# Optimization experiments

Measured on AMD Instinct MI355X. Metric: run time of the kernel, lower is better.

The kernel has to match this reference:

```python
import jax, jax.numpy as jnp
import numpy as np

H, E, NI = 100000, 200000, 1000000
D_H, D_E, D_OUT = 128, 64, 128
LN_EPS = 1e-5


def _linear(x, W, b):
    # torch nn.Linear convention: W is [out, in]
    return x @ W.T + b


def _scatter_mean(vals, idx, num_segments):
    # scatter_mean with empty segments producing 0 (sum=0 / max(count,1))
    s = jax.ops.segment_sum(vals, idx, num_segments=num_segments)
    c = jax.ops.segment_sum(jnp.ones((vals.shape[0], 1), vals.dtype), idx,
                            num_segments=num_segments)
    return s / jnp.maximum(c, 1.0)


def setup_inputs() -> dict:
    key = jax.random.key(0)
    ks = jax.random.split(key, 16)
    inv = lambda n: 1.0 / np.sqrt(n)
    return {
        "x_h": jax.random.normal(ks[0], (H, D_H), jnp.float32),
        "h2_edge_attr": jax.random.normal(ks[1], (E, D_E), jnp.float32),
        "Wp": jax.random.uniform(ks[2], (D_OUT, D_H), jnp.float32, -inv(D_H), inv(D_H)),
        "bp": jnp.zeros((D_OUT,), jnp.float32),
        "We1": jax.random.uniform(ks[3], (D_OUT, D_H + D_E), jnp.float32, -inv(D_H + D_E), inv(D_H + D_E)),
        "be1": jnp.zeros((D_OUT,), jnp.float32),
        "We2": jax.random.uniform(ks[4], (D_OUT, D_OUT), jnp.float32, -inv(D_OUT), inv(D_OUT)),
        "be2": jnp.zeros((D_OUT,), jnp.float32),
        "Wn1": jax.random.uniform(ks[5], (D_OUT, D_OUT), jnp.float32, -inv(D_OUT), inv(D_OUT)),
        "bn1": jnp.zeros((D_OUT,), jnp.float32),
        "Wn2": jax.random.uniform(ks[6], (D_OUT, D_OUT), jnp.float32, -inv(D_OUT), inv(D_OUT)),
        "bn2": jnp.zeros((D_OUT,), jnp.float32),
        "gamma": jnp.ones((D_OUT,), jnp.float32),
        "beta": jnp.zeros((D_OUT,), jnp.float32),
        "fg_id": jax.random.randint(ks[7], (NI,), 0, H, jnp.int32),
        "res_id": jax.random.randint(ks[8], (NI,), 0, E, jnp.int32),
    }


def reference(x_h, h2_edge_attr, Wp, bp, We1, be1, We2, be2,
              Wn1, bn1, Wn2, bn2, gamma, beta, fg_id, res_id):
    # node -> edge: mean of member node features per hyperedge
    edge_node_mean = _scatter_mean(x_h[fg_id], res_id, E)            # [E, d_h]
    e_in = jnp.concatenate([edge_node_mean, h2_edge_attr], axis=-1)  # [E, d_h+d_e]
    edge_msg = _linear(jax.nn.relu(_linear(e_in, We1, be1)), We2, be2)  # [E, d_out]
    # edge -> node: mean of incident edge messages per hypernode
    node_msg = _scatter_mean(edge_msg[res_id], fg_id, H)             # [H, d_out]
    z = _linear(x_h, Wp, bp) + _linear(jax.nn.relu(_linear(node_msg, Wn1, bn1)), Wn2, bn2)
    z = jax.nn.relu(z)
    mu = jnp.mean(z, axis=-1, keepdims=True)
    var = jnp.var(z, axis=-1, keepdims=True)
    return (z - mu) * jax.lax.rsqrt(var + LN_EPS) * gamma + beta
```

## Files before the change

kernel.cpp:

```cpp
#include <hip/hip_runtime.h>

#define H_N   100000
#define E_N   200000
#define NI_N  1000000
#define LN_EPS 1e-5f

#define NBUCK_E 3125
#define NBUCK_H 1563
#define SUBCAP_E 128
#define SUBCAP_H 192
#define CAP_E 512
#define CAP_H 1024
#define BCNT_PAD 16

typedef __attribute__((ext_vector_type(8))) short bf16x8;
typedef __attribute__((ext_vector_type(4))) float floatx4;
typedef __attribute__((ext_vector_type(4))) int intx4;

__device__ inline unsigned short f2bf(float f) {
  unsigned u = __builtin_bit_cast(unsigned, f);
  u += 0x7fffu + ((u >> 16) & 1u);
  return (unsigned short)(u >> 16);
}
__device__ inline float bf2f(unsigned short s) {
  unsigned u = ((unsigned)s) << 16;
  return __builtin_bit_cast(float, u);
}
__device__ inline unsigned get_xcc() {
  unsigned x;
  asm volatile("s_getreg_b32 %0, hwreg(HW_REG_XCC_ID)" : "=s"(x));
  return x & 7;
}

__global__ __launch_bounds__(256) void k_cvt_bf16(const float4* __restrict__ src,
                                                  unsigned short* __restrict__ dst,
                                                  int n4) {
  int i = blockIdx.x * 256 + threadIdx.x;
  if (i >= n4) return;
  float4 v = src[i];
  union { unsigned short us[4]; unsigned long long u64; } p;
  p.us[0] = f2bf(v.x); p.us[1] = f2bf(v.y);
  p.us[2] = f2bf(v.z); p.us[3] = f2bf(v.w);
  *(unsigned long long*)(dst + (size_t)i * 4) = p.u64;
}

__global__ __launch_bounds__(256) void k_bucket(
    const int* __restrict__ fg, const int* __restrict__ res,
    int* __restrict__ bcnt_e, int* __restrict__ bcnt_h,
    unsigned* __restrict__ pairs_e, unsigned* __restrict__ pairs_h) {
  int i0 = (blockIdx.x * 256 + threadIdx.x) * 4;
  if (i0 >= NI_N) return;
  unsigned xcc = get_xcc();
  intx4 f4 = __builtin_nontemporal_load((const intx4*)(fg + i0));
  intx4 r4 = __builtin_nontemporal_load((const intx4*)(res + i0));
#pragma unroll
  for (int j = 0; j < 4; ++j) {
    int f = f4[j], r = r4[j];
    int be = r >> 6, se = r & 63;
    int pe = atomicAdd(bcnt_e + ((size_t)xcc * NBUCK_E + be) * BCNT_PAD, 1);
    if (pe < SUBCAP_E)
      pairs_e[((size_t)xcc * NBUCK_E + be) * SUBCAP_E + pe] =
          ((unsigned)se << 24) | (unsigned)f;
    int bh = f >> 6, sh = f & 63;
    int ph = atomicAdd(bcnt_h + ((size_t)xcc * NBUCK_H + bh) * BCNT_PAD, 1);
    if (ph < SUBCAP_H)
      pairs_h[((size_t)xcc * NBUCK_H + bh) * SUBCAP_H + ph] =
          ((unsigned)sh << 24) | (unsigned)r;
  }
}

__global__ __launch_bounds__(256, 4) void k_edge_fused(
    const unsigned short* __restrict__ xh, const short* __restrict__ attr_bf,
    const unsigned* __restrict__ pairs, const int* __restrict__ bcnt,
    const short* __restrict__ w1, const float* __restrict__ b1,
    const short* __restrict__ w2, const float* __restrict__ b2,
    unsigned short* __restrict__ edge_msg) {
  __shared__ short meanS[64][136];
  __shared__ int ubuf[4352];
  short (*h1s)[136] = (short(*)[136])ubuf;
  unsigned* raw = (unsigned*)ubuf;
  unsigned* sortedp = raw + CAP_E;
  int* cnts = (int*)(sortedp + CAP_E);
  int* curs = cnts + 65;

  const int b = blockIdx.x;
  const int t = threadIdx.x;

  int total = 0;
#pragma unroll
  for (int x = 0; x < 8; ++x) {
    int c = min(bcnt[((size_t)x * NBUCK_E + b) * BCNT_PAD], SUBCAP_E);
    const unsigned* src = pairs + ((size_t)x * NBUCK_E + b) * SUBCAP_E;
    for (int j = t; j < c; j += 256) {
      int d = total + j;
      if (d < CAP_E) raw[d] = src[j];
    }
    total += c;
  }
  const int cnt = min(total, CAP_E);
  if (t <= 64) cnts[t] = 0;
  __syncthreads();
  for (int j = t; j < cnt; j += 256)
    atomicAdd(&cnts[(raw[j] >> 24) + 1], 1);
  __syncthreads();
  for (int d = 1; d <= 64; d <<= 1) {
    int v = 0;
    if (t <= 64 && t >= d) v = cnts[t - d];
    __syncthreads();
    if (t <= 64) cnts[t] += v;
    __syncthreads();
  }
  if (t < 64) curs[t] = cnts[t];
  __syncthreads();
  for (int j = t; j < cnt; j += 256) {
    unsigned p = raw[j];
    int d = atomicAdd(&curs[p >> 24], 1);
    sortedp[d] = p & 0xFFFFFFu;
  }
  __syncthreads();

  const int wave = t >> 6, lane = t & 63;
  for (int s = wave; s < 64; s += 4) {
    int o = cnts[s], e = cnts[s + 1];
    float a0 = 0.f, a1 = 0.f;
    int j = o;
    for (; j + 1 < e; j += 2) {
      int i0 = sortedp[j], i1 = sortedp[j + 1];
      unsigned v0 = *(const unsigned*)(xh + (size_t)i0 * 128 + lane * 2);
      unsigned v1 = *(const unsigned*)(xh + (size_t)i1 * 128 + lane * 2);
      a0 += bf2f((unsigned short)(v0 & 0xffffu)) + bf2f((unsigned short)(v1 & 0xffffu));
      a1 += bf2f((unsigned short)(v0 >> 16)) + bf2f((unsigned short)(v1 >> 16));
    }
    if (j < e) {
      int i0 = sortedp[j];
      unsigned v0 = *(const unsigned*)(xh + (size_t)i0 * 128 + lane * 2);
      a0 += bf2f((unsigned short)(v0 & 0xffffu));
      a1 += bf2f((unsigned short)(v0 >> 16));
    }
    float inv = (e > o) ? 1.0f / (float)(e - o) : 0.0f;
    *(unsigned*)&meanS[s][lane * 2] =
        (unsigned)f2bf(a0 * inv) | ((unsigned)f2bf(a1 * inv) << 16);
  }
  __syncthreads();

  const int row  = lane & 15;
  const int quad = lane >> 4;
  const int e0   = b * 64;
  const int cb   = wave * 32;

  bf16x8 B1[2][6];
#pragma unroll
  for (int nl = 0; nl < 2; ++nl)
#pragma unroll
    for (int ks = 0; ks < 6; ++ks)
      B1[nl][ks] = *(const bf16x8*)(w1 + (size_t)(cb + nl * 16 + row) * 192 +
                                    ks * 32 + quad * 8);

  floatx4 acc[4][2];
#pragma unroll
  for (int m = 0; m < 4; ++m)
#pragma unroll
    for (int nl = 0; nl < 2; ++nl) acc[m][nl] = (floatx4){0.f, 0.f, 0.f, 0.f};

#pragma unroll
  for (int ks = 0; ks < 6; ++ks) {
    bf16x8 a[4];
#pragma unroll
    for (int m = 0; m < 4; ++m) {
      if (ks < 4) {
        a[m] = *(const bf16x8*)&meanS[m * 16 + row][ks * 32 + quad * 8];
      } else {
        int e = e0 + m * 16 + row;
        a[m] = *(const bf16x8*)(attr_bf + (size_t)e * 64 + (ks - 4) * 32 + quad * 8);
      }
    }
#pragma unroll
    for (int m = 0; m < 4; ++m)
#pragma unroll
      for (int nl = 0; nl < 2; ++nl)
        acc[m][nl] = __builtin_amdgcn_mfma_f32_16x16x32_bf16(a[m], B1[nl][ks],
                                                             acc[m][nl], 0, 0, 0);
  }

#pragma unroll
  for (int nl = 0; nl < 2; ++nl) {
    float bias = b1[cb + nl * 16 + row];
#pragma unroll
    for (int m = 0; m < 4; ++m)
#pragma unroll
      for (int r = 0; r < 4; ++r)
        h1s[m * 16 + quad * 4 + r][cb + nl * 16 + row] =
            (short)f2bf(fmaxf(acc[m][nl][r] + bias, 0.0f));
  }

  bf16x8 B2[2][4];
#pragma unroll
  for (int nl = 0; nl < 2; ++nl)
#pragma unroll
    for (int ks = 0; ks < 4; ++ks)
      B2[nl][ks] = *(const bf16x8*)(w2 + (size_t)(cb + nl * 16 + row) * 128 +
                                    ks * 32 + quad * 8);
  __syncthreads();

  floatx4 acc2[4][2];
#pragma unroll
  for (int m = 0; m < 4; ++m)
#pragma unroll
    for (int nl = 0; nl < 2; ++nl) acc2[m][nl] = (floatx4){0.f, 0.f, 0.f, 0.f};

#pragma unroll
  for (int ks = 0; ks < 4; ++ks) {
    bf16x8 a[4];
#pragma unroll
    for (int m = 0; m < 4; ++m)
      a[m] = *(const bf16x8*)&h1s[m * 16 + row][ks * 32 + quad * 8];
#pragma unroll
    for (int m = 0; m < 4; ++m)
#pragma unroll
      for (int nl = 0; nl < 2; ++nl)
        acc2[m][nl] = __builtin_amdgcn_mfma_f32_16x16x32_bf16(a[m], B2[nl][ks],
                                                              acc2[m][nl], 0, 0, 0);
  }

#pragma unroll
  for (int nl = 0; nl < 2; ++nl) {
    int col = cb + nl * 16 + row;
    float bias = b2[col];
#pragma unroll
    for (int m = 0; m < 4; ++m)
#pragma unroll
      for (int r = 0; r < 4; ++r)
        edge_msg[(size_t)(e0 + m * 16 + quad * 4 + r) * 128 + col] =
            f2bf(acc2[m][nl][r] + bias);
  }
}

__global__ __launch_bounds__(256, 3) void k_node_fused(
    const unsigned short* __restrict__ emsg, const short* __restrict__ xh_bf,
    const unsigned* __restrict__ pairs, const int* __restrict__ bcnt,
    const short* __restrict__ wp, const float* __restrict__ bp,
    const short* __restrict__ wn1, const float* __restrict__ bn1,
    const short* __restrict__ wn2, const float* __restrict__ bn2,
    const float* __restrict__ gamma, const float* __restrict__ beta,
    float* __restrict__ out) {
  __shared__ short meanS[64][136];
  __shared__ int ubuf[4352];
  __shared__ float2 part[64][4];
  short (*h1s)[136] = (short(*)[136])ubuf;
  unsigned* raw = (unsigned*)ubuf;
  unsigned* sortedp = raw + CAP_H;
  int* cnts = (int*)(sortedp + CAP_H);
  int* curs = cnts + 65;

  const int b = blockIdx.x;
  const int t = threadIdx.x;

  int total = 0;
#pragma unroll
  for (int x = 0; x < 8; ++x) {
    int c = min(bcnt[((size_t)x * NBUCK_H + b) * BCNT_PAD], SUBCAP_H);
    const unsigned* src = pairs + ((size_t)x * NBUCK_H + b) * SUBCAP_H;
    for (int j = t; j < c; j += 256) {
      int d = total + j;
      if (d < CAP_H) raw[d] = src[j];
    }
    total += c;
  }
  const int cnt = min(total, CAP_H);
  if (t <= 64) cnts[t] = 0;
  __syncthreads();
  for (int j = t; j < cnt; j += 256)
    atomicAdd(&cnts[(raw[j] >> 24) + 1], 1);
  __syncthreads();
  for (int d = 1; d <= 64; d <<= 1) {
    int v = 0;
    if (t <= 64 && t >= d) v = cnts[t - d];
    __syncthreads();
    if (t <= 64) cnts[t] += v;
    __syncthreads();
  }
  if (t < 64) curs[t] = cnts[t];
  __syncthreads();
  for (int j = t; j < cnt; j += 256) {
    unsigned p = raw[j];
    int d = atomicAdd(&curs[p >> 24], 1);
    sortedp[d] = p & 0xFFFFFFu;
  }
  __syncthreads();

  const int wave = t >> 6, lane = t & 63;
  const int segs_here = min(64, H_N - b * 64);
  for (int s = wave; s < 64; s += 4) {
    if (s < segs_here) {
      int o = cnts[s], e = cnts[s + 1];
      float a0 = 0.f, a1 = 0.f;
      int j = o;
      for (; j + 1 < e; j += 2) {
        int i0 = sortedp[j], i1 = sortedp[j + 1];
        unsigned v0 = *(const unsigned*)(emsg + (size_t)i0 * 128 + lane * 2);
        unsigned v1 = *(const unsigned*)(emsg + (size_t)i1 * 128 + lane * 2);
        a0 += bf2f((unsigned short)(v0 & 0xffffu)) + bf2f((unsigned short)(v1 & 0xffffu));
        a1 += bf2f((unsigned short)(v0 >> 16)) + bf2f((unsigned short)(v1 >> 16));
      }
      if (j < e) {
        int i0 = sortedp[j];
        unsigned v0 = *(const unsigned*)(emsg + (size_t)i0 * 128 + lane * 2);
        a0 += bf2f((unsigned short)(v0 & 0xffffu));
        a1 += bf2f((unsigned short)(v0 >> 16));
      }
      float inv = (e > o) ? 1.0f / (float)(e - o) : 0.0f;
      *(unsigned*)&meanS[s][lane * 2] =
          (unsigned)f2bf(a0 * inv) | ((unsigned)f2bf(a1 * inv) << 16);
    } else {
      *(unsigned*)&meanS[s][lane * 2] = 0u;
    }
  }
  __syncthreads();

  const int row  = lane & 15;
  const int quad = lane >> 4;
  const int n0   = b * 64;
  const int cb   = wave * 32;

  bf16x8 B1[2][4];
#pragma unroll
  for (int nl = 0; nl < 2; ++nl)
#pragma unroll
    for (int ks = 0; ks < 4; ++ks)
      B1[nl][ks] = *(const bf16x8*)(wn1 + (size_t)(cb + nl * 16 + row) * 128 +
                                    ks * 32 + quad * 8);

  floatx4 acc[4][2];
#pragma unroll
  for (int m = 0; m < 4; ++m)
#pragma unroll
    for (int nl = 0; nl < 2; ++nl) acc[m][nl] = (floatx4){0.f, 0.f, 0.f, 0.f};

#pragma unroll
  for (int ks = 0; ks < 4; ++ks) {
    bf16x8 a[4];
#pragma unroll
    for (int m = 0; m < 4; ++m)
      a[m] = *(const bf16x8*)&meanS[m * 16 + row][ks * 32 + quad * 8];
#pragma unroll
    for (int m = 0; m < 4; ++m)
#pragma unroll
      for (int nl = 0; nl < 2; ++nl)
        acc[m][nl] = __builtin_amdgcn_mfma_f32_16x16x32_bf16(a[m], B1[nl][ks],
                                                             acc[m][nl], 0, 0, 0);
  }

#pragma unroll
  for (int nl = 0; nl < 2; ++nl) {
    float bias = bn1[cb + nl * 16 + row];
#pragma unroll
    for (int m = 0; m < 4; ++m)
#pragma unroll
      for (int r = 0; r < 4; ++r)
        h1s[m * 16 + quad * 4 + r][cb + nl * 16 + row] =
            (short)f2bf(fmaxf(acc[m][nl][r] + bias, 0.0f));
  }

  bf16x8 B2[2][4], Bp[2][4];
#pragma unroll
  for (int nl = 0; nl < 2; ++nl)
#pragma unroll
    for (int ks = 0; ks < 4; ++ks) {
      B2[nl][ks] = *(const bf16x8*)(wn2 + (size_t)(cb + nl * 16 + row) * 128 +
                                    ks * 32 + quad * 8);
      Bp[nl][ks] = *(const bf16x8*)(wp + (size_t)(cb + nl * 16 + row) * 128 +
                                    ks * 32 + quad * 8);
    }
  __syncthreads();

  floatx4 acc2[4][2];
#pragma unroll
  for (int m = 0; m < 4; ++m)
#pragma unroll
    for (int nl = 0; nl < 2; ++nl) acc2[m][nl] = (floatx4){0.f, 0.f, 0.f, 0.f};

#pragma unroll
  for (int ks = 0; ks < 4; ++ks) {
    bf16x8 at[4], ax[4];
#pragma unroll
    for (int m = 0; m < 4; ++m) {
      at[m] = *(const bf16x8*)&h1s[m * 16 + row][ks * 32 + quad * 8];
      int n = n0 + m * 16 + row;
      ax[m] = *(const bf16x8*)(xh_bf + (size_t)n * 128 + ks * 32 + quad * 8);
    }
#pragma unroll
    for (int m = 0; m < 4; ++m)
#pragma unroll
      for (int nl = 0; nl < 2; ++nl) {
        acc2[m][nl] = __builtin_amdgcn_mfma_f32_16x16x32_bf16(at[m], B2[nl][ks],
                                                              acc2[m][nl], 0, 0, 0);
        acc2[m][nl] = __builtin_amdgcn_mfma_f32_16x16x32_bf16(ax[m], Bp[nl][ks],
                                                              acc2[m][nl], 0, 0, 0);
      }
  }

  float z[4][2][4];
#pragma unroll
  for (int m = 0; m < 4; ++m) {
    float s[4], ss[4];
#pragma unroll
    for (int r = 0; r < 4; ++r) { s[r] = 0.f; ss[r] = 0.f; }
#pragma unroll
    for (int nl = 0; nl < 2; ++nl) {
      float bias = bp[cb + nl * 16 + row] + bn2[cb + nl * 16 + row];
#pragma unroll
      for (int r = 0; r < 4; ++r) {
        float v = fmaxf(acc2[m][nl][r] + bias, 0.0f);
        z[m][nl][r] = v;
        s[r] += v;
        ss[r] += v * v;
      }
    }
#pragma unroll
    for (int r = 0; r < 4; ++r) {
#pragma unroll
      for (int msk = 1; msk < 16; msk <<= 1) {
        s[r]  += __shfl_xor(s[r],  msk, 64);
        ss[r] += __shfl_xor(ss[r], msk, 64);
      }
      if (row == 0) part[m * 16 + quad * 4 + r][wave] = make_float2(s[r], ss[r]);
    }
  }
  __syncthreads();

#pragma unroll
  for (int m = 0; m < 4; ++m)
#pragma unroll
    for (int r = 0; r < 4; ++r) {
      int rr = m * 16 + quad * 4 + r;
      float2 p0 = part[rr][0], p1 = part[rr][1], p2 = part[rr][2], p3 = part[rr][3];
      float mean = (p0.x + p1.x + p2.x + p3.x) * (1.0f / 128.0f);
      float var  = (p0.y + p1.y + p2.y + p3.y) * (1.0f / 128.0f) - mean * mean;
      float rstd = rsqrtf(var + LN_EPS);
      int n = n0 + rr;
      if (n < H_N) {
#pragma unroll
        for (int nl = 0; nl < 2; ++nl) {
          int col = cb + nl * 16 + row;
          out[(size_t)n * 128 + col] =
              (z[m][nl][r] - mean) * rstd * gamma[col] + beta[col];
        }
      }
    }
}

extern "C" void kernel_launch(void* const* d_in, const int* in_sizes, int n_in,
                              void* d_out, int out_size, void* d_ws, size_t ws_size,
                              hipStream_t stream) {
  const float* x_h   = (const float*)d_in[0];
  const float* attr  = (const float*)d_in[1];
  const float* Wp    = (const float*)d_in[2];
  const float* bp    = (const float*)d_in[3];
  const float* We1   = (const float*)d_in[4];
  const float* be1   = (const float*)d_in[5];
  const float* We2   = (const float*)d_in[6];
  const float* be2   = (const float*)d_in[7];
  const float* Wn1   = (const float*)d_in[8];
  const float* bn1   = (const float*)d_in[9];
  const float* Wn2   = (const float*)d_in[10];
  const float* bn2   = (const float*)d_in[11];
  const float* gamma = (const float*)d_in[12];
  const float* beta  = (const float*)d_in[13];
  const int*   fg    = (const int*)d_in[14];
  const int*   res   = (const int*)d_in[15];
  float* out = (float*)d_out;

  int* bcnt_e = (int*)d_ws;
  int* bcnt_h = bcnt_e + (size_t)8 * NBUCK_E * BCNT_PAD;
  unsigned* pairs_e = (unsigned*)(bcnt_h + (size_t)8 * NBUCK_H * BCNT_PAD);
  unsigned* pairs_h = pairs_e + (size_t)8 * NBUCK_E * SUBCAP_E;
  unsigned short* xh_bf    = (unsigned short*)(pairs_h + (size_t)8 * NBUCK_H * SUBCAP_H);
  unsigned short* edge_msg = xh_bf + (size_t)H_N * 128;
  short* w1  = (short*)(edge_msg + (size_t)E_N * 128);
  short* w2  = w1 + 128 * 192;
  short* wn1 = w2 + 128 * 128;
  short* wn2 = wn1 + 128 * 128;
  short* wp  = wn2 + 128 * 128;
  short* attr_bf = wp + 128 * 128;

  hipMemsetAsync(bcnt_e, 0,
                 (size_t)(8 * NBUCK_E + 8 * NBUCK_H) * BCNT_PAD * 4, stream);

  {
    int n4 = H_N * 128 / 4;
    k_cvt_bf16<<<(n4 + 255) / 256, 256, 0, stream>>>((const float4*)x_h, xh_bf, n4);
    n4 = E_N * 64 / 4;
    k_cvt_bf16<<<(n4 + 255) / 256, 256, 0, stream>>>((const float4*)attr, (unsigned short*)attr_bf, n4);
    n4 = 128 * 192 / 4;
    k_cvt_bf16<<<(n4 + 255) / 256, 256, 0, stream>>>((const float4*)We1, (unsigned short*)w1, n4);
    n4 = 128 * 128 / 4;
    k_cvt_bf16<<<(n4 + 255) / 256, 256, 0, stream>>>((const float4*)We2, (unsigned short*)w2, n4);
    k_cvt_bf16<<<(n4 + 255) / 256, 256, 0, stream>>>((const float4*)Wn1, (unsigned short*)wn1, n4);
    k_cvt_bf16<<<(n4 + 255) / 256, 256, 0, stream>>>((const float4*)Wn2, (unsigned short*)wn2, n4);
    k_cvt_bf16<<<(n4 + 255) / 256, 256, 0, stream>>>((const float4*)Wp, (unsigned short*)wp, n4);
  }

  k_bucket<<<(NI_N / 4 + 255) / 256, 256, 0, stream>>>(fg, res, bcnt_e, bcnt_h,
                                                       pairs_e, pairs_h);

  k_edge_fused<<<NBUCK_E, 256, 0, stream>>>(xh_bf, attr_bf, pairs_e, bcnt_e,
                                            w1, be1, w2, be2, edge_msg);
  k_node_fused<<<NBUCK_H, 256, 0, stream>>>(edge_msg, (const short*)xh_bf,
                                            pairs_h, bcnt_h,
                                            wp, bp, wn1, bn1, wn2, bn2,
                                            gamma, beta, out);
}
```

Measured before the change: 529.6 us.

## Split gather waves into two half-rows with 8-byte loads and shrink LDS

The segment-mean gathers in both fused kernels now give each half-wave a different member row and have each lane load 8 bytes, then combine the halves with a cross-lane shuffle. Sorted indices are stored as precomputed byte offsets so the address math per load is cheaper. LDS is reorganised so the hidden activations reuse the mean buffer, guarded by an added barrier, and the kernels declare higher occupancy in their launch bounds. This aims to raise memory-level parallelism and occupancy in the latency-bound gather phase, at the cost of an extra sync and possible register pressure from the tighter launch bounds.

Result: faster. 481.7 us (-9.0%).

```diff
diff --git a/kernel.cpp b/kernel.cpp
--- a/kernel.cpp
+++ b/kernel.cpp
@@ -69,19 +69,18 @@
   }
 }
 
-__global__ __launch_bounds__(256, 4) void k_edge_fused(
+__global__ __launch_bounds__(256, 6) void k_edge_fused(
     const unsigned short* __restrict__ xh, const short* __restrict__ attr_bf,
     const unsigned* __restrict__ pairs, const int* __restrict__ bcnt,
     const short* __restrict__ w1, const float* __restrict__ b1,
     const short* __restrict__ w2, const float* __restrict__ b2,
     unsigned short* __restrict__ edge_msg) {
   __shared__ short meanS[64][136];
-  __shared__ int ubuf[4352];
-  short (*h1s)[136] = (short(*)[136])ubuf;
-  unsigned* raw = (unsigned*)ubuf;
-  unsigned* sortedp = raw + CAP_E;
-  int* cnts = (int*)(sortedp + CAP_E);
-  int* curs = cnts + 65;
+  __shared__ unsigned raw[CAP_E];
+  __shared__ unsigned sortedp[CAP_E];
+  __shared__ int cnts[65];
+  __shared__ int curs[64];
+  short (*h1s)[136] = meanS;
 
   const int b = blockIdx.x;
   const int t = threadIdx.x;
@@ -115,31 +114,43 @@
   for (int j = t; j < cnt; j += 256) {
     unsigned p = raw[j];
     int d = atomicAdd(&curs[p >> 24], 1);
-    sortedp[d] = p & 0xFFFFFFu;
+    sortedp[d] = (p & 0xFFFFFFu) << 8;
   }
   __syncthreads();
 
   const int wave = t >> 6, lane = t & 63;
+  const int half = lane >> 5, hl = lane & 31;
   for (int s = wave; s < 64; s += 4) {
     int o = cnts[s], e = cnts[s + 1];
-    float a0 = 0.f, a1 = 0.f;
-    int j = o;
-    for (; j + 1 < e; j += 2) {
-      int i0 = sortedp[j], i1 = sortedp[j + 1];
-      unsigned v0 = *(const unsigned*)(xh + (size_t)i0 * 128 + lane * 2);
-      unsigned v1 = *(const unsigned*)(xh + (size_t)i1 * 128 + lane * 2);
-      a0 += bf2f((unsigned short)(v0 & 0xffffu)) + bf2f((unsigned short)(v1 & 0xffffu));
-      a1 += bf2f((unsigned short)(v0 >> 16)) + bf2f((unsigned short)(v1 >> 16));
+    float a0 = 0.f, a1 = 0.f, a2 = 0.f, a3 = 0.f;
+    int j = o + half;
+    for (; j + 2 < e; j += 4) {
+      unsigned off0 = sortedp[j];
+      unsigned off1 = sortedp[j + 2];
+      uint2 v0 = *(const uint2*)((const char*)xh + off0 + hl * 8);
+      uint2 v1 = *(const uint2*)((const char*)xh + off1 + hl * 8);
+      a0 += bf2f((unsigned short)(v0.x & 0xffffu)) + bf2f((unsigned short)(v1.x & 0xffffu));
+      a1 += bf2f((unsigned short)(v0.x >> 16))     + bf2f((unsigned short)(v1.x >> 16));
+      a2 += bf2f((unsigned short)(v0.y & 0xffffu)) + bf2f((unsigned short)(v1.y & 0xffffu));
+      a3 += bf2f((unsigned short)(v0.y >> 16))     + bf2f((unsigned short)(v1.y >> 16));
     }
     if (j < e) {
-      int i0 = sortedp[j];
-      unsigned v0 = *(const unsigned*)(xh + (size_t)i0 * 128 + lane * 2);
-      a0 += bf2f((unsigned short)(v0 & 0xffffu));
-      a1 += bf2f((unsigned short)(v0 >> 16));
-    }
-    float inv = (e > o) ? 1.0f / (float)(e - o) : 0.0f;
-    *(unsigned*)&meanS[s][lane * 2] =
-        (unsigned)f2bf(a0 * inv) | ((unsigned)f2bf(a1 * inv) << 16);
+      unsigned off0 = sortedp[j];
+      uint2 v0 = *(const uint2*)((const char*)xh + off0 + hl * 8);
+      a0 += bf2f((unsigned short)(v0.x & 0xffffu));
+      a1 += bf2f((unsigned short)(v0.x >> 16));
+      a2 += bf2f((unsigned short)(v0.y & 0xffffu));
+      a3 += bf2f((unsigned short)(v0.y >> 16));
+    }
+    a0 += __shfl_xor(a0, 32); a1 += __shfl_xor(a1, 32);
+    a2 += __shfl_xor(a2, 32); a3 += __shfl_xor(a3, 32);
+    if (half == 0) {
+      float inv = (e > o) ? 1.0f / (float)(e - o) : 0.0f;
+      uint2 ov;
+      ov.x = (unsigned)f2bf(a0 * inv) | ((unsigned)f2bf(a1 * inv) << 16);
+      ov.y = (unsigned)f2bf(a2 * inv) | ((unsigned)f2bf(a3 * inv) << 16);
+      *(uint2*)&meanS[s][hl * 4] = ov;
+    }
   }
   __syncthreads();
 
@@ -181,6 +192,7 @@
         acc[m][nl] = __builtin_amdgcn_mfma_f32_16x16x32_bf16(a[m], B1[nl][ks],
                                                              acc[m][nl], 0, 0, 0);
   }
+  __syncthreads();
 
 #pragma unroll
   for (int nl = 0; nl < 2; ++nl) {
@@ -235,7 +247,7 @@
   }
 }
 
-__global__ __launch_bounds__(256, 3) void k_node_fused(
+__global__ __launch_bounds__(256, 5) void k_node_fused(
     const unsigned short* __restrict__ emsg, const short* __restrict__ xh_bf,
     const unsigned* __restrict__ pairs, const int* __restrict__ bcnt,
     const short* __restrict__ wp, const float* __restrict__ bp,
@@ -244,13 +256,12 @@
     const float* __restrict__ gamma, const float* __restrict__ beta,
     float* __restrict__ out) {
   __shared__ short meanS[64][136];
-  __shared__ int ubuf[4352];
-  __shared__ float2 part[64][4];
-  short (*h1s)[136] = (short(*)[136])ubuf;
-  unsigned* raw = (unsigned*)ubuf;
-  unsigned* sortedp = raw + CAP_H;
-  int* cnts = (int*)(sortedp + CAP_H);
-  int* curs = cnts + 65;
+  __shared__ unsigned raw[CAP_H];
+  __shared__ unsigned sortedp[CAP_H];
+  __shared__ int cnts[65];
+  __shared__ int curs[64];
+  short (*h1s)[136] = meanS;
+  float2 (*part)[4] = (float2(*)[4])raw;
 
   const int b = blockIdx.x;
   const int t = threadIdx.x;
@@ -284,35 +295,44 @@
   for (int j = t; j < cnt; j += 256) {
     unsigned p = raw[j];
     int d = atomicAdd(&curs[p >> 24], 1);
-    sortedp[d] = p & 0xFFFFFFu;
+    sortedp[d] = (p & 0xFFFFFFu) << 8;
   }
   __syncthreads();
 
   const int wave = t >> 6, lane = t & 63;
+  const int half = lane >> 5, hl = lane & 31;
   const int segs_here = min(64, H_N - b * 64);
   for (int s = wave; s < 64; s += 4) {
-    if (s < segs_here) {
-      int o = cnts[s], e = cnts[s + 1];
-      float a0 = 0.f, a1 = 0.f;
-      int j = o;
-      for (; j + 1 < e; j += 2) {
-        int i0 = sortedp[j], i1 = sortedp[j + 1];
-        unsigned v0 = *(const unsigned*)(emsg + (size_t)i0 * 128 + lane * 2);
-        unsigned v1 = *(const unsigned*)(emsg + (size_t)i1 * 128 + lane * 2);
-        a0 += bf2f((unsigned short)(v0 & 0xffffu)) + bf2f((unsigned short)(v1 & 0xffffu));
-        a1 += bf2f((unsigned short)(v0 >> 16)) + bf2f((unsigned short)(v1 >> 16));
-      }
-      if (j < e) {
-        int i0 = sortedp[j];
-        unsigned v0 = *(const unsigned*)(emsg + (size_t)i0 * 128 + lane * 2);
-        a0 += bf2f((unsigned short)(v0 & 0xffffu));
-        a1 += bf2f((unsigned short)(v0 >> 16));
-      }
+    int o = 0, e = 0;
+    if (s < segs_here) { o = cnts[s]; e = cnts[s + 1]; }
+    float a0 = 0.f, a1 = 0.f, a2 = 0.f, a3 = 0.f;
+    int j = o + half;
+    for (; j + 2 < e; j += 4) {
+      unsigned off0 = sortedp[j];
+      unsigned off1 = sortedp[j + 2];
+      uint2 v0 = *(const uint2*)((const char*)emsg + off0 + hl * 8);
+      uint2 v1 = *(const uint2*)((const char*)emsg + off1 + hl * 8);
+      a0 += bf2f((unsigned short)(v0.x & 0xffffu)) + bf2f((unsigned short)(v1.x & 0xffffu));
+      a1 += bf2f((unsigned short)(v0.x >> 16))     + bf2f((unsigned short)(v1.x >> 16));
+      a2 += bf2f((unsigned short)(v0.y & 0xffffu)) + bf2f((unsigned short)(v1.y & 0xffffu));
+      a3 += bf2f((unsigned short)(v0.y >> 16))     + bf2f((unsigned short)(v1.y >> 16));
+    }
+    if (j < e) {
+      unsigned off0 = sortedp[j];
+      uint2 v0 = *(const uint2*)((const char*)emsg + off0 + hl * 8);
+      a0 += bf2f((unsigned short)(v0.x & 0xffffu));
+      a1 += bf2f((unsigned short)(v0.x >> 16));
+      a2 += bf2f((unsigned short)(v0.y & 0xffffu));
+      a3 += bf2f((unsigned short)(v0.y >> 16));
+    }
+    a0 += __shfl_xor(a0, 32); a1 += __shfl_xor(a1, 32);
+    a2 += __shfl_xor(a2, 32); a3 += __shfl_xor(a3, 32);
+    if (half == 0) {
       float inv = (e > o) ? 1.0f / (float)(e - o) : 0.0f;
-      *(unsigned*)&meanS[s][lane * 2] =
-          (unsigned)f2bf(a0 * inv) | ((unsigned)f2bf(a1 * inv) << 16);
-    } else {
-      *(unsigned*)&meanS[s][lane * 2] = 0u;
+      uint2 ov;
+      ov.x = (unsigned)f2bf(a0 * inv) | ((unsigned)f2bf(a1 * inv) << 16);
+      ov.y = (unsigned)f2bf(a2 * inv) | ((unsigned)f2bf(a3 * inv) << 16);
+      *(uint2*)&meanS[s][hl * 4] = ov;
     }
   }
   __syncthreads();
@@ -349,6 +369,7 @@
         acc[m][nl] = __builtin_amdgcn_mfma_f32_16x16x32_bf16(a[m], B1[nl][ks],
                                                              acc[m][nl], 0, 0, 0);
   }
+  __syncthreads();
 
 #pragma unroll
   for (int nl = 0; nl < 2; ++nl) {
```

## Replace per-block segment sort with LDS float atomic accumulation in fused kernels

Applied to the files above, without the earlier changes.

Both fused edge and node kernels drop the in-block counting sort (prefix scan plus scatter into a sorted list). Each wave now walks the raw pair list directly and accumulates gathered rows into an fp32 LDS accumulator with atomicAdd, while per-segment counts are kept separately. The mean and the bf16 conversion move into the MFMA A-fragment load. This removes several barriers and the sorting pass and spreads gather work evenly across waves instead of per segment, at the cost of many LDS float atomics with possible contention. Because LDS is reorganised, the node kernel's occupancy hint also rises from 3 to 4 blocks.

Result: slower. 1.739 ms (+228.4%).

```diff
diff --git a/kernel.cpp b/kernel.cpp
--- a/kernel.cpp
+++ b/kernel.cpp
@@ -30,6 +30,12 @@
   unsigned x;
   asm volatile("s_getreg_b32 %0, hwreg(HW_REG_XCC_ID)" : "=s"(x));
   return x & 7;
+}
+__device__ inline bf16x8 cvt_frag(const float* p, float inv) {
+  bf16x8 r;
+#pragma unroll
+  for (int i = 0; i < 8; ++i) r[i] = (short)f2bf(p[i] * inv);
+  return r;
 }
 
 __global__ __launch_bounds__(256) void k_cvt_bf16(const float4* __restrict__ src,
@@ -75,16 +81,16 @@
     const short* __restrict__ w1, const float* __restrict__ b1,
     const short* __restrict__ w2, const float* __restrict__ b2,
     unsigned short* __restrict__ edge_msg) {
-  __shared__ short meanS[64][136];
-  __shared__ int ubuf[4352];
-  short (*h1s)[136] = (short(*)[136])ubuf;
-  unsigned* raw = (unsigned*)ubuf;
-  unsigned* sortedp = raw + CAP_E;
-  int* cnts = (int*)(sortedp + CAP_E);
-  int* curs = cnts + 65;
+  __shared__ float accS[64][132];
+  __shared__ unsigned raw[CAP_E];
+  __shared__ int cnts[64];
+  short (*h1s)[136] = (short(*)[136])accS;
 
   const int b = blockIdx.x;
   const int t = threadIdx.x;
+
+  for (int i = t; i < 64 * 132; i += 256) ((float*)accS)[i] = 0.f;
+  if (t < 64) cnts[t] = 0;
 
   int total = 0;
 #pragma unroll
@@ -98,48 +104,38 @@
     total += c;
   }
   const int cnt = min(total, CAP_E);
-  if (t <= 64) cnts[t] = 0;
-  __syncthreads();
+  __syncthreads();
+
   for (int j = t; j < cnt; j += 256)
-    atomicAdd(&cnts[(raw[j] >> 24) + 1], 1);
-  __syncthreads();
-  for (int d = 1; d <= 64; d <<= 1) {
-    int v = 0;
-    if (t <= 64 && t >= d) v = cnts[t - d];
-    __syncthreads();
-    if (t <= 64) cnts[t] += v;
-    __syncthreads();
-  }
-  if (t < 64) curs[t] = cnts[t];
-  __syncthreads();
-  for (int j = t; j < cnt; j += 256) {
-    unsigned p = raw[j];
-    int d = atomicAdd(&curs[p >> 24], 1);
-    sortedp[d] = p & 0xFFFFFFu;
-  }
-  __syncthreads();
+    atomicAdd(&cnts[raw[j] >> 24], 1);
 
   const int wave = t >> 6, lane = t & 63;
-  for (int s = wave; s < 64; s += 4) {
-    int o = cnts[s], e = cnts[s + 1];
-    float a0 = 0.f, a1 = 0.f;
-    int j = o;
-    for (; j + 1 < e; j += 2) {
-      int i0 = sortedp[j], i1 = sortedp[j + 1];
-      unsigned v0 = *(const unsigned*)(xh + (size_t)i0 * 128 + lane * 2);
-      unsigned v1 = *(const unsigned*)(xh + (size_t)i1 * 128 + lane * 2);
-      a0 += bf2f((unsigned short)(v0 & 0xffffu)) + bf2f((unsigned short)(v1 & 0xffffu));
-      a1 += bf2f((unsigned short)(v0 >> 16)) + bf2f((unsigned short)(v1 >> 16));
-    }
-    if (j < e) {
-      int i0 = sortedp[j];
-      unsigned v0 = *(const unsigned*)(xh + (size_t)i0 * 128 + lane * 2);
-      a0 += bf2f((unsigned short)(v0 & 0xffffu));
-      a1 += bf2f((unsigned short)(v0 >> 16));
-    }
-    float inv = (e > o) ? 1.0f / (float)(e - o) : 0.0f;
-    *(unsigned*)&meanS[s][lane * 2] =
-        (unsigned)f2bf(a0 * inv) | ((unsigned)f2bf(a1 * inv) << 16);
+  {
+    const char* base = (const char*)xh;
+    int j = wave;
+    for (; j + 12 < cnt; j += 16) {
+      unsigned p0 = raw[j], p1 = raw[j + 4], p2 = raw[j + 8], p3 = raw[j + 12];
+      unsigned v0 = *(const unsigned*)(base + ((size_t)(p0 & 0xFFFFFFu) << 8) + lane * 4);
+      unsigned v1 = *(const unsigned*)(base + ((size_t)(p1 & 0xFFFFFFu) << 8) + lane * 4);
+      unsigned v2 = *(const unsigned*)(base + ((size_t)(p2 & 0xFFFFFFu) << 8) + lane * 4);
+      unsigned v3 = *(const unsigned*)(base + ((size_t)(p3 & 0xFFFFFFu) << 8) + lane * 4);
+      int s0 = p0 >> 24, s1 = p1 >> 24, s2 = p2 >> 24, s3 = p3 >> 24;
+      atomicAdd(&accS[s0][lane * 2],     bf2f((unsigned short)(v0 & 0xffffu)));
+      atomicAdd(&accS[s0][lane * 2 + 1], bf2f((unsigned short)(v0 >> 16)));
+      atomicAdd(&accS[s1][lane * 2],     bf2f((unsigned short)(v1 & 0xffffu)));
+      atomicAdd(&accS[s1][lane * 2 + 1], bf2f((unsigned short)(v1 >> 16)));
+      atomicAdd(&accS[s2][lane * 2],     bf2f((unsigned short)(v2 & 0xffffu)));
+      atomicAdd(&accS[s2][lane * 2 + 1], bf2f((unsigned short)(v2 >> 16)));
+      atomicAdd(&accS[s3][lane * 2],     bf2f((unsigned short)(v3 & 0xffffu)));
+      atomicAdd(&accS[s3][lane * 2 + 1], bf2f((unsigned short)(v3 >> 16)));
+    }
+    for (; j < cnt; j += 4) {
+      unsigned p0 = raw[j];
+      unsigned v0 = *(const unsigned*)(base + ((size_t)(p0 & 0xFFFFFFu) << 8) + lane * 4);
+      int s0 = p0 >> 24;
+      atomicAdd(&accS[s0][lane * 2],     bf2f((unsigned short)(v0 & 0xffffu)));
+      atomicAdd(&accS[s0][lane * 2 + 1], bf2f((unsigned short)(v0 >> 16)));
+    }
   }
   __syncthreads();
 
@@ -148,6 +144,13 @@
   const int e0   = b * 64;
   const int cb   = wave * 32;
 
+  float invr[4];
+#pragma unroll
+  for (int m = 0; m < 4; ++m) {
+    int c = cnts[m * 16 + row];
+    invr[m] = c > 0 ? 1.0f / (float)c : 0.0f;
+  }
+
   bf16x8 B1[2][6];
 #pragma unroll
   for (int nl = 0; nl < 2; ++nl)
@@ -168,7 +171,7 @@
 #pragma unroll
     for (int m = 0; m < 4; ++m) {
       if (ks < 4) {
-        a[m] = *(const bf16x8*)&meanS[m * 16 + row][ks * 32 + quad * 8];
+        a[m] = cvt_frag(&accS[m * 16 + row][ks * 32 + quad * 8], invr[m]);
       } else {
         int e = e0 + m * 16 + row;
         a[m] = *(const bf16x8*)(attr_bf + (size_t)e * 64 + (ks - 4) * 32 + quad * 8);
@@ -181,6 +184,7 @@
         acc[m][nl] = __builtin_amdgcn_mfma_f32_16x16x32_bf16(a[m], B1[nl][ks],
                                                              acc[m][nl], 0, 0, 0);
   }
+  __syncthreads();
 
 #pragma unroll
   for (int nl = 0; nl < 2; ++nl) {
@@ -235,7 +239,7 @@
   }
 }
 
-__global__ __launch_bounds__(256, 3) void k_node_fused(
+__global__ __launch_bounds__(256, 4) void k_node_fused(
     const unsigned short* __restrict__ emsg, const short* __restrict__ xh_bf,
     const unsigned* __restrict__ pairs, const int* __restrict__ bcnt,
     const short* __restrict__ wp, const float* __restrict__ bp,
@@ -243,17 +247,17 @@
     const short* __restrict__ wn2, const float* __restrict__ bn2,
     const float* __restrict__ gamma, const float* __restrict__ beta,
     float* __restrict__ out) {
-  __shared__ short meanS[64][136];
-  __shared__ int ubuf[4352];
-  __shared__ float2 part[64][4];
-  short (*h1s)[136] = (short(*)[136])ubuf;
-  unsigned* raw = (unsigned*)ubuf;
-  unsigned* sortedp = raw + CAP_H;
-  int* cnts = (int*)(sortedp + CAP_H);
-  int* curs = cnts + 65;
+  __shared__ float accS[64][132];
+  __shared__ unsigned raw[CAP_H];
+  __shared__ int cnts[64];
+  short (*h1s)[136] = (short(*)[136])accS;
+  float2 (*part)[4] = (float2(*)[4])raw;
 
   const int b = blockIdx.x;
   const int t = threadIdx.x;
+
+  for (int i = t; i < 64 * 132; i += 256) ((float*)accS)[i] = 0.f;
+  if (t < 64) cnts[t] = 0;
 
   int total = 0;
 #pragma unroll
@@ -267,52 +271,37 @@
     total += c;
   }
   const int cnt = min(total, CAP_H);
-  if (t <= 64) cnts[t] = 0;
-  __syncthreads();
+  __syncthreads();
+
   for (int j = t; j < cnt; j += 256)
-    atomicAdd(&cnts[(raw[j] >> 24) + 1], 1);
-  __syncthreads();
-  for (int d = 1; d <= 64; d <<= 1) {
-    int v = 0;
-    if (t <= 64 && t >= d) v = cnts[t - d];
-    __syncthreads();
-    if (t <= 64) cnts[t] += v;
-    __syncthreads();
-  }
-  if (t < 64) curs[t] = cnts[t];
-  __syncthreads();
-  for (int j = t; j < cnt; j += 256) {
-    unsigned p = raw[j];
-    int d = atomicAdd(&curs[p >> 24], 1);
-    sortedp[d] = p & 0xFFFFFFu;
-  }
-  __syncthreads();
+    atomicAdd(&cnts[raw[j] >> 24], 1);
 
   const int wave = t >> 6, lane = t & 63;
-  const int segs_here = min(64, H_N - b * 64);
-  for (int s = wave; s < 64; s += 4) {
-    if (s < segs_here) {
-      int o = cnts[s], e = cnts[s + 1];
-      float a0 = 0.f, a1 = 0.f;
-      int j = o;
-      for (; j + 1 < e; j += 2) {
-        int i0 = sortedp[j], i1 = sortedp[j + 1];
-        unsigned v0 = *(const unsigned*)(emsg + (size_t)i0 * 128 + lane * 2);
-        unsigned v1 = *(const unsigned*)(emsg + (size_t)i1 * 128 + lane * 2);
-        a0 += bf2f((unsigned short)(v0 & 0xffffu)) + bf2f((unsigned short)(v1 & 0xffffu));
-        a1 += bf2f((unsigned short)(v0 >> 16)) + bf2f((unsigned short)(v1 >> 16));
-      }
-      if (j < e) {
-        int i0 = sortedp[j];
-        unsigned v0 = *(const unsigned*)(emsg + (size_t)i0 * 128 + lane * 2);
-        a0 += bf2f((unsigned short)(v0 & 0xffffu));
-        a1 += bf2f((unsigned short)(v0 >> 16));
-      }
-      float inv = (e > o) ? 1.0f / (float)(e - o) : 0.0f;
-      *(unsigned*)&meanS[s][lane * 2] =
-          (unsigned)f2bf(a0 * inv) | ((unsigned)f2bf(a1 * inv) << 16);
-    } else {
-      *(unsigned*)&meanS[s][lane * 2] = 0u;
+  {
+    const char* base = (const char*)emsg;
+    int j = wave;
+    for (; j + 12 < cnt; j += 16) {
+      unsigned p0 = raw[j], p1 = raw[j + 4], p2 = raw[j + 8], p3 = raw[j + 12];
+      unsigned v0 = *(const unsigned*)(base + ((size_t)(p0 & 0xFFFFFFu) << 8) + lane * 4);
+      unsigned v1 = *(const unsigned*)(base + ((size_t)(p1 & 0xFFFFFFu) << 8) + lane * 4);
+      unsigned v2 = *(const unsigned*)(base + ((size_t)(p2 & 0xFFFFFFu) << 8) + lane * 4);
+      unsigned v3 = *(const unsigned*)(base + ((size_t)(p3 & 0xFFFFFFu) << 8) + lane * 4);
+      int s0 = p0 >> 24, s1 = p1 >> 24, s2 = p2 >> 24, s3 = p3 >> 24;
+      atomicAdd(&accS[s0][lane * 2],     bf2f((unsigned short)(v0 & 0xffffu)));
+      atomicAdd(&accS[s0][lane * 2 + 1], bf2f((unsigned short)(v0 >> 16)));
+      atomicAdd(&accS[s1][lane * 2],     bf2f((unsigned short)(v1 & 0xffffu)));
+      atomicAdd(&accS[s1][lane * 2 + 1], bf2f((unsigned short)(v1 >> 16)));
+      atomicAdd(&accS[s2][lane * 2],     bf2f((unsigned short)(v2 & 0xffffu)));
+      atomicAdd(&accS[s2][lane * 2 + 1], bf2f((unsigned short)(v2 >> 16)));
+      atomicAdd(&accS[s3][lane * 2],     bf2f((unsigned short)(v3 & 0xffffu)));
+      atomicAdd(&accS[s3][lane * 2 + 1], bf2f((unsigned short)(v3 >> 16)));
+    }
+    for (; j < cnt; j += 4) {
+      unsigned p0 = raw[j];
+      unsigned v0 = *(const unsigned*)(base + ((size_t)(p0 & 0xFFFFFFu) << 8) + lane * 4);
+      int s0 = p0 >> 24;
+      atomicAdd(&accS[s0][lane * 2],     bf2f((unsigned short)(v0 & 0xffffu)));
+      atomicAdd(&accS[s0][lane * 2 + 1], bf2f((unsigned short)(v0 >> 16)));
     }
   }
   __syncthreads();
@@ -322,6 +311,13 @@
   const int n0   = b * 64;
   const int cb   = wave * 32;
 
+  float invr[4];
+#pragma unroll
+  for (int m = 0; m < 4; ++m) {
+    int c = cnts[m * 16 + row];
+    invr[m] = c > 0 ? 1.0f / (float)c : 0.0f;
+  }
+
   bf16x8 B1[2][4];
 #pragma unroll
   for (int nl = 0; nl < 2; ++nl)
@@ -341,7 +337,7 @@
     bf16x8 a[4];
 #pragma unroll
     for (int m = 0; m < 4; ++m)
-      a[m] = *(const bf16x8*)&meanS[m * 16 + row][ks * 32 + quad * 8];
+      a[m] = cvt_frag(&accS[m * 16 + row][ks * 32 + quad * 8], invr[m]);
 #pragma unroll
     for (int m = 0; m < 4; ++m)
 #pragma unroll
@@ -349,6 +345,7 @@
         acc[m][nl] = __builtin_amdgcn_mfma_f32_16x16x32_bf16(a[m], B1[nl][ks],
                                                              acc[m][nl], 0, 0, 0);
   }
+  __syncthreads();
 
 #pragma unroll
   for (int nl = 0; nl < 2; ++nl) {
```

## Balance segment gathers across waves with run-based fp32 LDS accumulation

Applied to the files above, without the earlier changes.

Both fused kernels previously gave each wave a fixed set of 16 segments, so per-segment counts could leave waves unevenly loaded. Now each wave takes an equal contiguous slice of the sorted pair list, issues 8 independent row loads at a time using pre-shifted byte offsets, and flushes partial sums per run into an fp32 LDS accumulator with LDS atomics. Division by the count and bf16 conversion move into the MFMA A-fragment load, and an extra barrier is added before the accumulator buffer is reused for h1. The cost is more LDS (a float accumulator instead of bf16), LDS atomics at run boundaries, and zero-initialising the accumulator.

Result: slower. 597.3 us (+12.8%).

```diff
diff --git a/kernel.cpp b/kernel.cpp
--- a/kernel.cpp
+++ b/kernel.cpp
@@ -12,6 +12,7 @@
 #define CAP_E 512
 #define CAP_H 1024
 #define BCNT_PAD 16
+#define GMASK 0x03FFFF00u
 
 typedef __attribute__((ext_vector_type(8))) short bf16x8;
 typedef __attribute__((ext_vector_type(4))) float floatx4;
@@ -30,6 +31,12 @@
   unsigned x;
   asm volatile("s_getreg_b32 %0, hwreg(HW_REG_XCC_ID)" : "=s"(x));
   return x & 7;
+}
+__device__ inline bf16x8 cvt_frag(const float* p, float inv) {
+  bf16x8 r;
+#pragma unroll
+  for (int i = 0; i < 8; ++i) r[i] = (short)f2bf(p[i] * inv);
+  return r;
 }
 
 __global__ __launch_bounds__(256) void k_cvt_bf16(const float4* __restrict__ src,
@@ -69,22 +76,73 @@
   }
 }
 
+#define GATHER_RUNS(basePtr)                                                   \
+  {                                                                            \
+    const char* base = (const char*)(basePtr);                                 \
+    int begin = (cnt * wave) >> 2;                                             \
+    int end   = (cnt * (wave + 1)) >> 2;                                       \
+    float a0 = 0.f, a1 = 0.f;                                                  \
+    int cur = -1;                                                              \
+    int j = begin;                                                             \
+    for (; j + 7 < end; j += 8) {                                              \
+      unsigned e[8]; unsigned v[8];                                            \
+      _Pragma("unroll")                                                        \
+      for (int u = 0; u < 8; ++u)                                              \
+        e[u] = (unsigned)__builtin_amdgcn_readfirstlane((int)sortedp[j + u]);  \
+      _Pragma("unroll")                                                        \
+      for (int u = 0; u < 8; ++u)                                              \
+        v[u] = *(const unsigned*)(base + (e[u] & GMASK) + lane * 4);           \
+      _Pragma("unroll")                                                        \
+      for (int u = 0; u < 8; ++u) {                                            \
+        int s = (int)(e[u] >> 26);                                             \
+        if (s != cur) {                                                        \
+          if (cur >= 0) {                                                      \
+            atomicAdd(&accS[cur][lane * 2], a0);                               \
+            atomicAdd(&accS[cur][lane * 2 + 1], a1);                           \
+          }                                                                    \
+          cur = s; a0 = 0.f; a1 = 0.f;                                         \
+        }                                                                      \
+        a0 += bf2f((unsigned short)(v[u] & 0xffffu));                          \
+        a1 += bf2f((unsigned short)(v[u] >> 16));                              \
+      }                                                                        \
+    }                                                                          \
+    for (; j < end; ++j) {                                                     \
+      unsigned e0 = (unsigned)__builtin_amdgcn_readfirstlane((int)sortedp[j]); \
+      unsigned v0 = *(const unsigned*)(base + (e0 & GMASK) + lane * 4);        \
+      int s = (int)(e0 >> 26);                                                 \
+      if (s != cur) {                                                          \
+        if (cur >= 0) {                                                        \
+          atomicAdd(&accS[cur][lane * 2], a0);                                 \
+          atomicAdd(&accS[cur][lane * 2 + 1], a1);                             \
+        }                                                                      \
+        cur = s; a0 = 0.f; a1 = 0.f;                                           \
+      }                                                                        \
+      a0 += bf2f((unsigned short)(v0 & 0xffffu));                              \
+      a1 += bf2f((unsigned short)(v0 >> 16));                                  \
+    }                                                                          \
+    if (cur >= 0) {                                                            \
+      atomicAdd(&accS[cur][lane * 2], a0);                                     \
+      atomicAdd(&accS[cur][lane * 2 + 1], a1);                                 \
+    }                                                                          \
+  }
+
 __global__ __launch_bounds__(256, 4) void k_edge_fused(
     const unsigned short* __restrict__ xh, const short* __restrict__ attr_bf,
     const unsigned* __restrict__ pairs, const int* __restrict__ bcnt,
     const short* __restrict__ w1, const float* __restrict__ b1,
     const short* __restrict__ w2, const float* __restrict__ b2,
     unsigned short* __restrict__ edge_msg) {
-  __shared__ short meanS[64][136];
-  __shared__ int ubuf[4352];
-  short (*h1s)[136] = (short(*)[136])ubuf;
-  unsigned* raw = (unsigned*)ubuf;
-  unsigned* sortedp = raw + CAP_E;
-  int* cnts = (int*)(sortedp + CAP_E);
-  int* curs = cnts + 65;
+  __shared__ float accS[64][132];
+  __shared__ unsigned raw[CAP_E];
+  __shared__ unsigned sortedp[CAP_E];
+  __shared__ int cnts[65];
+  __shared__ int curs[64];
+  short (*h1s)[136] = (short(*)[136])accS;
 
   const int b = blockIdx.x;
   const int t = threadIdx.x;
+
+  for (int i = t; i < 64 * 132; i += 256) ((float*)accS)[i] = 0.f;
 
   int total = 0;
 #pragma unroll
@@ -115,32 +173,12 @@
   for (int j = t; j < cnt; j += 256) {
     unsigned p = raw[j];
     int d = atomicAdd(&curs[p >> 24], 1);
-    sortedp[d] = p & 0xFFFFFFu;
+    sortedp[d] = ((p >> 24) << 26) | ((p & 0xFFFFFFu) << 8);
   }
   __syncthreads();
 
   const int wave = t >> 6, lane = t & 63;
-  for (int s = wave; s < 64; s += 4) {
-    int o = cnts[s], e = cnts[s + 1];
-    float a0 = 0.f, a1 = 0.f;
-    int j = o;
-    for (; j + 1 < e; j += 2) {
-      int i0 = sortedp[j], i1 = sortedp[j + 1];
-      unsigned v0 = *(const unsigned*)(xh + (size_t)i0 * 128 + lane * 2);
-      unsigned v1 = *(const unsigned*)(xh + (size_t)i1 * 128 + lane * 2);
-      a0 += bf2f((unsigned short)(v0 & 0xffffu)) + bf2f((unsigned short)(v1 & 0xffffu));
-      a1 += bf2f((unsigned short)(v0 >> 16)) + bf2f((unsigned short)(v1 >> 16));
-    }
-    if (j < e) {
-      int i0 = sortedp[j];
-      unsigned v0 = *(const unsigned*)(xh + (size_t)i0 * 128 + lane * 2);
-      a0 += bf2f((unsigned short)(v0 & 0xffffu));
-      a1 += bf2f((unsigned short)(v0 >> 16));
-    }
-    float inv = (e > o) ? 1.0f / (float)(e - o) : 0.0f;
-    *(unsigned*)&meanS[s][lane * 2] =
-        (unsigned)f2bf(a0 * inv) | ((unsigned)f2bf(a1 * inv) << 16);
-  }
+  GATHER_RUNS(xh);
   __syncthreads();
 
   const int row  = lane & 15;
@@ -148,6 +186,14 @@
   const int e0   = b * 64;
   const int cb   = wave * 32;
 
+  float invr[4];
+#pragma unroll
+  for (int m = 0; m < 4; ++m) {
+    int s = m * 16 + row;
+    int c = cnts[s + 1] - cnts[s];
+    invr[m] = c > 0 ? 1.0f / (float)c : 0.0f;
+  }
+
   bf16x8 B1[2][6];
 #pragma unroll
   for (int nl = 0; nl < 2; ++nl)
@@ -168,7 +214,7 @@
 #pragma unroll
     for (int m = 0; m < 4; ++m) {
       if (ks < 4) {
-        a[m] = *(const bf16x8*)&meanS[m * 16 + row][ks * 32 + quad * 8];
+        a[m] = cvt_frag(&accS[m * 16 + row][ks * 32 + quad * 8], invr[m]);
       } else {
         int e = e0 + m * 16 + row;
         a[m] = *(const bf16x8*)(attr_bf + (size_t)e * 64 + (ks - 4) * 32 + quad * 8);
@@ -181,6 +227,7 @@
         acc[m][nl] = __builtin_amdgcn_mfma_f32_16x16x32_bf16(a[m], B1[nl][ks],
                                                              acc[m][nl], 0, 0, 0);
   }
+  __syncthreads();
 
 #pragma unroll
   for (int nl = 0; nl < 2; ++nl) {
@@ -243,17 +290,18 @@
     const short* __restrict__ wn2, const float* __restrict__ bn2,
     const float* __restrict__ gamma, const float* __restrict__ beta,
     float* __restrict__ out) {
-  __shared__ short meanS[64][136];
-  __shared__ int ubuf[4352];
-  __shared__ float2 part[64][4];
-  short (*h1s)[136] = (short(*)[136])ubuf;
-  unsigned* raw = (unsigned*)ubuf;
-  unsigned* sortedp = raw + CAP_H;
-  int* cnts = (int*)(sortedp + CAP_H);
-  int* curs = cnts + 65;
+  __shared__ float accS[64][132];
+  __shared__ unsigned raw[CAP_H];
+  __shared__ unsigned sortedp[CAP_H];
+  __shared__ int cnts[65];
+  __shared__ int curs[64];
+  short (*h1s)[136] = (short(*)[136])accS;
+  float2 (*part)[4] = (float2(*)[4])raw;
 
   const int b = blockIdx.x;
   const int t = threadIdx.x;
+
+  for (int i = t; i < 64 * 132; i += 256) ((float*)accS)[i] = 0.f;
 
   int total = 0;
 #pragma unroll
@@ -284,37 +332,12 @@
   for (int j = t; j < cnt; j += 256) {
     unsigned p = raw[j];
     int d = atomicAdd(&curs[p >> 24], 1);
-    sortedp[d] = p & 0xFFFFFFu;
+    sortedp[d] = ((p >> 24) << 26) | ((p & 0xFFFFFFu) << 8);
   }
   __syncthreads();
 
   const int wave = t >> 6, lane = t & 63;
-  const int segs_here = min(64, H_N - b * 64);
-  for (int s = wave; s < 64; s += 4) {
-    if (s < segs_here) {
-      int o = cnts[s], e = cnts[s + 1];
-      float a0 = 0.f, a1 = 0.f;
-      int j = o;
-      for (; j + 1 < e; j += 2) {
-        int i0 = sortedp[j], i1 = sortedp[j + 1];
-        unsigned v0 = *(const unsigned*)(emsg + (size_t)i0 * 128 + lane * 2);
-        unsigned v1 = *(const unsigned*)(emsg + (size_t)i1 * 128 + lane * 2);
-        a0 += bf2f((unsigned short)(v0 & 0xffffu)) + bf2f((unsigned short)(v1 & 0xffffu));
-        a1 += bf2f((unsigned short)(v0 >> 16)) + bf2f((unsigned short)(v1 >> 16));
-      }
-      if (j < e) {
-        int i0 = sortedp[j];
-        unsigned v0 = *(const unsigned*)(emsg + (size_t)i0 * 128 + lane * 2);
-        a0 += bf2f((unsigned short)(v0 & 0xffffu));
-        a1 += bf2f((unsigned short)(v0 >> 16));
-      }
-      float inv = (e > o) ? 1.0f / (float)(e - o) : 0.0f;
-      *(unsigned*)&meanS[s][lane * 2] =
-          (unsigned)f2bf(a0 * inv) | ((unsigned)f2bf(a1 * inv) << 16);
-    } else {
-      *(unsigned*)&meanS[s][lane * 2] = 0u;
-    }
-  }
+  GATHER_RUNS(emsg);
   __syncthreads();
 
   const int row  = lane & 15;
@@ -322,6 +345,14 @@
   const int n0   = b * 64;
   const int cb   = wave * 32;
 
+  float invr[4];
+#pragma unroll
+  for (int m = 0; m < 4; ++m) {
+    int s = m * 16 + row;
+    int c = cnts[s + 1] - cnts[s];
+    invr[m] = c > 0 ? 1.0f / (float)c : 0.0f;
+  }
+
   bf16x8 B1[2][4];
 #pragma unroll
   for (int nl = 0; nl < 2; ++nl)
@@ -341,7 +372,7 @@
     bf16x8 a[4];
 #pragma unroll
     for (int m = 0; m < 4; ++m)
-      a[m] = *(const bf16x8*)&meanS[m * 16 + row][ks * 32 + quad * 8];
+      a[m] = cvt_frag(&accS[m * 16 + row][ks * 32 + quad * 8], invr[m]);
 #pragma unroll
     for (int m = 0; m < 4; ++m)
 #pragma unroll
@@ -349,6 +380,7 @@
         acc[m][nl] = __builtin_amdgcn_mfma_f32_16x16x32_bf16(a[m], B1[nl][ks],
                                                              acc[m][nl], 0, 0, 0);
   }
+  __syncthreads();
 
 #pragma unroll
   for (int nl = 0; nl < 2; ++nl) {
```
